# Kernel tuning notes

Measured on AMD Instinct MI355X. Metric: run time of the kernel, lower is better.

The kernel has to match this reference:

```python
import jax, jax.numpy as jnp
import numpy as np

EMBED_DIM = 1024
NUM_HEADS = 16
HEAD_DIM = EMBED_DIM // NUM_HEADS

# Hamilton-product combination tensor C[out_comp, weight_comp, in_comp]
_C = np.zeros((4, 4, 4), dtype=np.float32)
for o, terms in enumerate([
    [(0, 0, 1), (1, 1, -1), (2, 2, -1), (3, 3, -1)],  # r_out
    [(1, 0, 1), (0, 1, 1), (3, 2, 1), (2, 3, -1)],    # i_out
    [(2, 0, 1), (3, 1, -1), (0, 2, 1), (1, 3, 1)],    # j_out
    [(3, 0, 1), (2, 1, 1), (1, 2, -1), (0, 3, 1)],    # k_out
]):
    for d, c, s in terms:
        _C[o, d, c] = s
C = jnp.asarray(_C)


def _xavier(key, shape):
    fan_in, fan_out = shape[-1], shape[-2]
    a = jnp.sqrt(6.0 / (fan_in + fan_out))
    return jax.random.uniform(key, shape, jnp.float32, -a, a)


def setup_inputs() -> dict:
    key = jax.random.key(0)
    ks = jax.random.split(key, 8)
    B, T, E = 4, 1024, EMBED_DIM
    inp = {
        'q': jax.random.normal(ks[0], (B, T, E, 4), jnp.float32),
        'k': jax.random.normal(ks[1], (B, T, E, 4), jnp.float32),
        'v': jax.random.normal(ks[2], (B, T, E, 4), jnp.float32),
    }
    for name, kk in zip(['Wq', 'Wk', 'Wv', 'Wo'], ks[3:7]):
        # stacked [r,i,j,k] weights, each (out_features, in_features)
        inp[name] = _xavier(kk, (4, E, E))
        inp[name.replace('W', 'b')] = jnp.zeros((E, 4), jnp.float32)
    return inp


def qlinear(x, W, b):
    # x: [B,T,in,4(c)], W: [4(d),out,in], b: [out,4]
    # effective block weight: Weff[q_out, c_in, out, in]
    Weff = jnp.einsum('doi,qdc->qcoi', W, C)
    out = jnp.einsum('btic,qcoi->btoq', x, Weff)
    return out + b  # bias broadcasts over B,T


def split_heads(x):
    B, T, D, Q = x.shape
    x = x.reshape(B, T, NUM_HEADS, HEAD_DIM, Q)
    return x.transpose(0, 2, 1, 3, 4)  # [B,H,T,hd,4]


def combine_heads(x):
    B, H, T, D, Q = x.shape
    return x.transpose(0, 2, 1, 3, 4).reshape(B, T, H * D, Q)


def reference(q, k, v, Wq, bq, Wk, bk, Wv, bv, Wo, bo):
    qh = split_heads(qlinear(q, Wq, bq))
    kh = split_heads(qlinear(k, Wk, bk))
    vh = split_heads(qlinear(v, Wv, bv))
    scale = 1.0 / jnp.sqrt(jnp.float32(HEAD_DIM * 4))
    scores = jnp.einsum('bhqfd,bhkfd->bhqk', qh, kh) * scale
    attn = jax.nn.softmax(scores, axis=-1)
    out = jnp.einsum('bhqk,bhkfd->bhqfd', attn, vh)
    return qlinear(combine_heads(out), Wo, bo)
```

## Files before the change

### kernel.cpp

```cpp
#include <hip/hip_runtime.h>
#include <hip/hip_bf16.h>

typedef _Float16 h16;
typedef h16   h16x8 __attribute__((ext_vector_type(8)));
typedef h16   h16x4 __attribute__((ext_vector_type(4)));
typedef float f32x4 __attribute__((ext_vector_type(4)));

#define EMB 1024
#define ED4 4096L

__device__ __forceinline__ void gload_lds16(const void* g, void* l) {
    __builtin_amdgcn_global_load_lds(
        (__attribute__((address_space(1))) void*)g,
        (__attribute__((address_space(3))) void*)l,
        16, 0, 0);
}

__global__ __launch_bounds__(256) void k_build_m(const float* __restrict__ W, h16* __restrict__ M) {
    int t = blockIdx.x * 256 + threadIdx.x;
    int i = t & 1023;
    int n = t >> 10;
    int o = n >> 2, q = n & 3;
    unsigned packed = 0xEu | (0x8u << 4) | (0x2u << 8) | (0x4u << 12);
    unsigned sm = (packed >> (q * 4)) & 0xFu;
    h16x4 out;
#pragma unroll
    for (int c = 0; c < 4; ++c) {
        int d = q ^ c;
        float w = W[((long)d * EMB + o) * EMB + i];
        out[c] = (h16)(((sm >> c) & 1u) ? -w : w);
    }
    *(h16x4*)&M[(long)n * ED4 + i * 4] = out;
}

__global__ __launch_bounds__(256) void k_f32_to_f16(const float* __restrict__ in, h16* __restrict__ out) {
    long i = ((long)blockIdx.x * 256 + threadIdx.x) * 4;
    float4 v = *(const float4*)(in + i);
    h16x4 o;
    o[0] = (h16)v.x; o[1] = (h16)v.y; o[2] = (h16)v.z; o[3] = (h16)v.w;
    *(h16x4*)(out + i) = o;
}

#define BAR() __builtin_amdgcn_s_barrier()
#define LGKM0() do { asm volatile("s_waitcnt lgkmcnt(0)" ::: "memory"); \
                     __builtin_amdgcn_sched_barrier(0); } while (0)
#define STAGE(matv, basev, row0v, tt, hh) do { \
    const h16* _src = (basev) + ((row0v) + (hh) * 128L) * 4096L + (long)(tt) * 64 + scol; \
    h16* _dst = &lds[(((tt) & 1) << 15) + (matv) * 16384 + (hh) * 8192 + w * 512]; \
    gload_lds16(_src, _dst); \
    gload_lds16(_src + 64 * 4096L, _dst + 4096); \
} while (0)
#define LDA_(m, ks) (*(const h16x8*)&lds[cb + wm * 8192 + ((m) * 16 + fr) * 64 + ((((ks) * 4 + kq) ^ fr7) << 3)])
#define LDB_(n, ks) (*(const h16x8*)&lds[cb + 16384 + (wn >> 1) * 8192 + (((wn & 1) * 64) + (n) * 16 + fr) * 64 + ((((ks) * 4 + kq) ^ fr7) << 3)])

template <typename OUT_T>
__global__ __launch_bounds__(512, 2) void k_gemm256(
    const h16* __restrict__ A, const h16* __restrict__ B,
    OUT_T* __restrict__ C, const float* __restrict__ bias, int nt)
{
    __shared__ __align__(16) h16 lds[65536];

    const int tid = threadIdx.x;
    const int w  = tid >> 6, l = tid & 63;
    const int wm = w >> 2, wn = w & 3;
    const int fr = l & 15, fr7 = l & 7, kq = l >> 4;

    const int srow = w * 8 + (l >> 3);
    const int scol = ((l & 7) ^ ((l >> 3) & 7)) << 3;
    const long arow0 = (long)blockIdx.x * 256 + srow;
    const long brow0 = (long)blockIdx.y * 256 + srow;

    f32x4 acc[8][4] = {};

    STAGE(0, A, arow0, 0, 0);
    STAGE(0, A, arow0, 0, 1);
    STAGE(1, B, brow0, 0, 0);
    STAGE(1, B, brow0, 0, 1);
    STAGE(0, A, arow0, 1, 0);
    STAGE(0, A, arow0, 1, 1);
    STAGE(1, B, brow0, 1, 0);
    STAGE(1, B, brow0, 1, 1);
    asm volatile("s_waitcnt vmcnt(8)" ::: "memory");
    __builtin_amdgcn_sched_barrier(0);
    BAR();

    for (int t = 0; t < nt; ++t) {
        const int cb = (t & 1) << 15;
        h16x8 alo[4][2], ahi[4][2], bf[4][2];

#pragma unroll
        for (int m = 0; m < 4; ++m) { alo[m][0] = LDA_(m, 0); alo[m][1] = LDA_(m, 1); }
#pragma unroll
        for (int n = 0; n < 2; ++n) { bf[n][0] = LDB_(n, 0); bf[n][1] = LDB_(n, 1); }
        BAR(); LGKM0();
        __builtin_amdgcn_s_setprio(1);
#pragma unroll
        for (int m = 0; m < 4; ++m)
#pragma unroll
            for (int n = 0; n < 2; ++n) {
                acc[m][n] = __builtin_amdgcn_mfma_f32_16x16x32_f16(alo[m][0], bf[n][0], acc[m][n], 0, 0, 0);
                acc[m][n] = __builtin_amdgcn_mfma_f32_16x16x32_f16(alo[m][1], bf[n][1], acc[m][n], 0, 0, 0);
            }
        __builtin_amdgcn_s_setprio(0);
        BAR();

#pragma unroll
        for (int n = 2; n < 4; ++n) { bf[n][0] = LDB_(n, 0); bf[n][1] = LDB_(n, 1); }
        BAR(); LGKM0();
        __builtin_amdgcn_s_setprio(1);
#pragma unroll
        for (int m = 0; m < 4; ++m)
#pragma unroll
            for (int n = 2; n < 4; ++n) {
                acc[m][n] = __builtin_amdgcn_mfma_f32_16x16x32_f16(alo[m][0], bf[n][0], acc[m][n], 0, 0, 0);
                acc[m][n] = __builtin_amdgcn_mfma_f32_16x16x32_f16(alo[m][1], bf[n][1], acc[m][n], 0, 0, 0);
            }
        __builtin_amdgcn_s_setprio(0);
        BAR();

#pragma unroll
        for (int m = 0; m < 4; ++m) { ahi[m][0] = LDA_(m + 4, 0); ahi[m][1] = LDA_(m + 4, 1); }
        if (t + 2 < nt) {
            STAGE(1, B, brow0, t + 2, 0);
            STAGE(1, B, brow0, t + 2, 1);
        }
        BAR(); LGKM0();
        __builtin_amdgcn_s_setprio(1);
#pragma unroll
        for (int m = 0; m < 4; ++m)
#pragma unroll
            for (int n = 0; n < 2; ++n) {
                acc[m + 4][n] = __builtin_amdgcn_mfma_f32_16x16x32_f16(ahi[m][0], bf[n][0], acc[m + 4][n], 0, 0, 0);
                acc[m + 4][n] = __builtin_amdgcn_mfma_f32_16x16x32_f16(ahi[m][1], bf[n][1], acc[m + 4][n], 0, 0, 0);
            }
        __builtin_amdgcn_s_setprio(0);
        BAR();

        if (t + 2 < nt) {
            STAGE(0, A, arow0, t + 2, 0);
            STAGE(0, A, arow0, t + 2, 1);
        }
        if (t < nt - 2)       { asm volatile("s_waitcnt vmcnt(8)" ::: "memory"); }
        else                  { asm volatile("s_waitcnt vmcnt(0)" ::: "memory"); }
        __builtin_amdgcn_sched_barrier(0);
        BAR();
        __builtin_amdgcn_s_setprio(1);
#pragma unroll
        for (int m = 0; m < 4; ++m)
#pragma unroll
            for (int n = 2; n < 4; ++n) {
                acc[m + 4][n] = __builtin_amdgcn_mfma_f32_16x16x32_f16(ahi[m][0], bf[n][0], acc[m + 4][n], 0, 0, 0);
                acc[m + 4][n] = __builtin_amdgcn_mfma_f32_16x16x32_f16(ahi[m][1], bf[n][1], acc[m + 4][n], 0, 0, 0);
            }
        __builtin_amdgcn_s_setprio(0);
        BAR();
    }

    const long row0 = (long)blockIdx.x * 256 + wm * 128 + kq * 4;
    const int  col0 = (int)blockIdx.y * 256 + wn * 64 + fr;
#pragma unroll
    for (int n = 0; n < 4; ++n) {
        const int col = col0 + n * 16;
        const float bv = bias[col];
#pragma unroll
        for (int m = 0; m < 8; ++m) {
#pragma unroll
            for (int j = 0; j < 4; ++j)
                C[(row0 + m * 16 + j) * 4096L + col] = (OUT_T)(acc[m][n][j] + bv);
        }
    }
}

template <typename OUT_T, bool HAS_BIAS>
__global__ __launch_bounds__(256) void k_gemm_bt(
    const h16* __restrict__ A, const h16* __restrict__ B,
    OUT_T* __restrict__ C, const float* __restrict__ bias,
    int lda, int ldb, int ldc,
    long sAb, long sAh, long sBb, long sBh, long sCb, long sCh,
    float alpha, int kIters)
{
    __shared__ __align__(16) h16 As[128 * 32];
    __shared__ __align__(16) h16 Bs[128 * 32];

    const int z = blockIdx.z, zb = z >> 4, zh = z & 15;
    const h16* Ab = A + zb * sAb + zh * sAh + (long)blockIdx.x * 128 * lda;
    const h16* Bb = B + zb * sBb + zh * sBh + (long)blockIdx.y * 128 * ldb;

    const int tid = threadIdx.x, w = tid >> 6, lane = tid & 63;
    const int wr = (w >> 1) * 64, wc = (w & 1) * 64;
    const int scol = (lane & 3) * 8;
    const int srow = lane >> 2;
    const int koff = (lane >> 4) * 8;
    const int fr   = lane & 15;

    f32x4 acc[4][4] = {};

    for (int kt = 0; kt < kIters; ++kt) {
        const int k0 = kt * 32;
#pragma unroll
        for (int j = 0; j < 2; ++j) {
            const int ca  = w * 2 + j;
            const int row = ca * 16 + srow;
            gload_lds16(Ab + (long)row * lda + k0 + scol, &As[ca * 512]);
            gload_lds16(Bb + (long)row * ldb + k0 + scol, &Bs[ca * 512]);
        }
        __syncthreads();

        h16x8 af[4], bfr[4];
#pragma unroll
        for (int m = 0; m < 4; ++m)
            af[m] = *(const h16x8*)&As[(wr + m * 16 + fr) * 32 + koff];
#pragma unroll
        for (int n = 0; n < 4; ++n)
            bfr[n] = *(const h16x8*)&Bs[(wc + n * 16 + fr) * 32 + koff];
        __syncthreads();

#pragma unroll
        for (int m = 0; m < 4; ++m)
#pragma unroll
            for (int n = 0; n < 4; ++n)
                acc[m][n] = __builtin_amdgcn_mfma_f32_16x16x32_f16(af[m], bfr[n], acc[m][n], 0, 0, 0);
    }

    OUT_T* Cb = C + zb * sCb + zh * sCh;
    const long rbase = (long)blockIdx.x * 128 + wr + (lane >> 4) * 4;
    const int  cbase = blockIdx.y * 128 + wc + fr;
#pragma unroll
    for (int n = 0; n < 4; ++n) {
        const int col = cbase + n * 16;
        const float bv = HAS_BIAS ? bias[col] : 0.0f;
#pragma unroll
        for (int m = 0; m < 4; ++m) {
            const long row0 = rbase + m * 16;
#pragma unroll
            for (int j = 0; j < 4; ++j) {
                float vv = acc[m][n][j] * alpha + bv;
                Cb[(row0 + j) * ldc + col] = (OUT_T)vv;
            }
        }
    }
}

__global__ void k_transpose_v(const h16* __restrict__ Vb, h16* __restrict__ Vt) {
    __shared__ h16 tile[32][34];
    const int z = blockIdx.z, b = z >> 4, h = z & 15;
    const int f0 = blockIdx.x * 32, t0 = blockIdx.y * 32;
    const int tx = threadIdx.x, ty = threadIdx.y;
#pragma unroll
    for (int j = 0; j < 4; ++j)
        tile[ty + 8 * j][tx] = Vb[(long)(b * 1024 + t0 + ty + 8 * j) * ED4 + h * 256 + f0 + tx];
    __syncthreads();
#pragma unroll
    for (int j = 0; j < 4; ++j)
        Vt[(long)z * (256 * 1024) + (long)(f0 + ty + 8 * j) * 1024 + t0 + tx] = tile[tx][ty + 8 * j];
}

__global__ __launch_bounds__(256) void k_softmax(h16* __restrict__ S) {
    const long row = blockIdx.x;
    h16* p = S + row * 1024;
    const int tid = threadIdx.x, w = tid >> 6, lane = tid & 63;
    h16x4 xi = *(const h16x4*)&p[tid * 4];
    float x[4];
#pragma unroll
    for (int j = 0; j < 4; ++j) x[j] = (float)xi[j];
    float m = fmaxf(fmaxf(x[0], x[1]), fmaxf(x[2], x[3]));
#pragma unroll
    for (int off = 32; off; off >>= 1) m = fmaxf(m, __shfl_xor(m, off));
    __shared__ float red[8];
    if (lane == 0) red[w] = m;
    __syncthreads();
    m = fmaxf(fmaxf(red[0], red[1]), fmaxf(red[2], red[3]));
    float s = 0.0f;
#pragma unroll
    for (int j = 0; j < 4; ++j) { x[j] = __expf(x[j] - m); s += x[j]; }
#pragma unroll
    for (int off = 32; off; off >>= 1) s += __shfl_xor(s, off);
    if (lane == 0) red[4 + w] = s;
    __syncthreads();
    s = red[4] + red[5] + red[6] + red[7];
    const float inv = 1.0f / s;
    h16x4 o;
#pragma unroll
    for (int j = 0; j < 4; ++j) o[j] = (h16)(x[j] * inv);
    *(h16x4*)&p[tid * 4] = o;
}

extern "C" void kernel_launch(void* const* d_in, const int* in_sizes, int n_in,
                              void* d_out, int out_size, void* d_ws, size_t ws_size,
                              hipStream_t stream) {
    const float* q  = (const float*)d_in[0];
    const float* k  = (const float*)d_in[1];
    const float* v  = (const float*)d_in[2];
    const float* Wq = (const float*)d_in[3];
    const float* bq = (const float*)d_in[4];
    const float* Wk = (const float*)d_in[5];
    const float* bk = (const float*)d_in[6];
    const float* Wv = (const float*)d_in[7];
    const float* bv = (const float*)d_in[8];
    const float* Wo = (const float*)d_in[9];
    const float* bo = (const float*)d_in[10];
    float* out = (float*)d_out;

    char* ws = (char*)d_ws;
    const long MB = 1024L * 1024;
    h16* X  = (h16*)(ws + 0 * MB);
    h16* M  = (h16*)(ws + 32 * MB);
    h16* Qb = (h16*)(ws + 64 * MB);
    h16* Kb = (h16*)(ws + 96 * MB);
    h16* Vb = (h16*)(ws + 128 * MB);
    h16* Vt = (h16*)(ws + 160 * MB);
    h16* AO = (h16*)(ws + 192 * MB);
    h16* Sc = (h16*)(ws + 224 * MB);

    dim3 blk(256);
    dim3 g256(16, 16, 1);

    k_f32_to_f16<<<16384, blk, 0, stream>>>(q, X);
    k_build_m<<<16384, blk, 0, stream>>>(Wq, M);
    k_gemm256<h16><<<g256, 512, 0, stream>>>(X, M, Qb, bq, 64);

    k_f32_to_f16<<<16384, blk, 0, stream>>>(k, X);
    k_build_m<<<16384, blk, 0, stream>>>(Wk, M);
    k_gemm256<h16><<<g256, 512, 0, stream>>>(X, M, Kb, bk, 64);

    k_f32_to_f16<<<16384, blk, 0, stream>>>(v, X);
    k_build_m<<<16384, blk, 0, stream>>>(Wv, M);
    k_gemm256<h16><<<g256, 512, 0, stream>>>(X, M, Vb, bv, 64);

    k_transpose_v<<<dim3(8, 32, 64), dim3(32, 8), 0, stream>>>(Vb, Vt);

    for (int c = 0; c < 4; ++c) {
        const h16* Qc  = Qb + (long)c * 1024 * 4096;
        const h16* Kc  = Kb + (long)c * 1024 * 4096;
        const h16* VtC = Vt + (long)c * 16 * 256 * 1024;
        h16*       AOc = AO + (long)c * 1024 * 4096;

        k_gemm_bt<h16, false><<<dim3(8, 8, 16), blk, 0, stream>>>(
            Qc, Kc, Sc, nullptr,
            4096, 4096, 1024,
            0, 256,
            0, 256,
            0, 1024L * 1024,
            0.0625f, 8);

        k_softmax<<<16384, blk, 0, stream>>>(Sc);

        k_gemm_bt<h16, false><<<dim3(8, 2, 16), blk, 0, stream>>>(
            Sc, VtC, AOc, nullptr,
            1024, 1024, 4096,
            0, 1024L * 1024,
            0, 256L * 1024,
            0, 256,
            1.0f, 32);
    }

    k_build_m<<<16384, blk, 0, stream>>>(Wo, M);
    k_gemm256<float><<<g256, 512, 0, stream>>>(AO, M, out, bo, 64);
}
```

Baseline: 917.9 us.

## Remap warp tiles to quadrant layout and stage half-tiles as soon as freed

Each warp's 128x64 output tile is re-laid out as four 64x32 quadrants, one in each 128-row A half and 128-column B half of the block tile. Each warp now reads only one A half and one B half at a time. The global-to-LDS loads are spread across the four MFMA phases, so each half-tile of the next stages is issued as soon as its LDS half is no longer needed, with a tighter vmcnt wait. The aim is finer overlap of loads with compute and fewer bursts of outstanding loads, at the cost of more complex buffer-reuse timing, where a hazard could corrupt data.

```diff
diff --git a/kernel.cpp b/kernel.cpp
--- a/kernel.cpp
+++ b/kernel.cpp
@@ -50,8 +50,19 @@
     gload_lds16(_src, _dst); \
     gload_lds16(_src + 64 * 4096L, _dst + 4096); \
 } while (0)
-#define LDA_(m, ks) (*(const h16x8*)&lds[cb + wm * 8192 + ((m) * 16 + fr) * 64 + ((((ks) * 4 + kq) ^ fr7) << 3)])
-#define LDB_(n, ks) (*(const h16x8*)&lds[cb + 16384 + (wn >> 1) * 8192 + (((wn & 1) * 64) + (n) * 16 + fr) * 64 + ((((ks) * 4 + kq) ^ fr7) << 3)])
+#define LDA_(mh, m, ks) (*(const h16x8*)&lds[cb + (mh) * 8192 + (wm * 64 + (m) * 16 + fr) * 64 + ((((ks) * 4 + kq) ^ fr7) << 3)])
+#define LDB_(nh, n, ks) (*(const h16x8*)&lds[cb + 16384 + (nh) * 8192 + (wn * 32 + (n) * 16 + fr) * 64 + ((((ks) * 4 + kq) ^ fr7) << 3)])
+#define MFMA_Q(MH, NH, BF) do { \
+    __builtin_amdgcn_s_setprio(1); \
+    _Pragma("unroll") \
+    for (int m = 0; m < 4; ++m) \
+        _Pragma("unroll") \
+        for (int n = 0; n < 2; ++n) { \
+            acc[MH][NH][m][n] = __builtin_amdgcn_mfma_f32_16x16x32_f16(af[m][0], BF[n][0], acc[MH][NH][m][n], 0, 0, 0); \
+            acc[MH][NH][m][n] = __builtin_amdgcn_mfma_f32_16x16x32_f16(af[m][1], BF[n][1], acc[MH][NH][m][n], 0, 0, 0); \
+        } \
+    __builtin_amdgcn_s_setprio(0); \
+} while (0)
 
 template <typename OUT_T>
 __global__ __launch_bounds__(512, 2) void k_gemm256(
@@ -70,105 +81,72 @@
     const long arow0 = (long)blockIdx.x * 256 + srow;
     const long brow0 = (long)blockIdx.y * 256 + srow;
 
-    f32x4 acc[8][4] = {};
+    f32x4 acc[2][2][4][2] = {};
 
     STAGE(0, A, arow0, 0, 0);
+    STAGE(1, B, brow0, 0, 0);
     STAGE(0, A, arow0, 0, 1);
-    STAGE(1, B, brow0, 0, 0);
     STAGE(1, B, brow0, 0, 1);
     STAGE(0, A, arow0, 1, 0);
-    STAGE(0, A, arow0, 1, 1);
     STAGE(1, B, brow0, 1, 0);
-    STAGE(1, B, brow0, 1, 1);
-    asm volatile("s_waitcnt vmcnt(8)" ::: "memory");
+    asm volatile("s_waitcnt vmcnt(4)" ::: "memory");
     __builtin_amdgcn_sched_barrier(0);
     BAR();
 
     for (int t = 0; t < nt; ++t) {
         const int cb = (t & 1) << 15;
-        h16x8 alo[4][2], ahi[4][2], bf[4][2];
-
-#pragma unroll
-        for (int m = 0; m < 4; ++m) { alo[m][0] = LDA_(m, 0); alo[m][1] = LDA_(m, 1); }
-#pragma unroll
-        for (int n = 0; n < 2; ++n) { bf[n][0] = LDB_(n, 0); bf[n][1] = LDB_(n, 1); }
+        h16x8 af[4][2], b0[2][2], b1[2][2];
+
+#pragma unroll
+        for (int m = 0; m < 4; ++m) { af[m][0] = LDA_(0, m, 0); af[m][1] = LDA_(0, m, 1); }
+#pragma unroll
+        for (int n = 0; n < 2; ++n) { b0[n][0] = LDB_(0, n, 0); b0[n][1] = LDB_(0, n, 1); }
+        if (t + 1 < nt) STAGE(0, A, arow0, t + 1, 1);
         BAR(); LGKM0();
-        __builtin_amdgcn_s_setprio(1);
-#pragma unroll
-        for (int m = 0; m < 4; ++m)
+        MFMA_Q(0, 0, b0);
+        BAR();
+
+#pragma unroll
+        for (int n = 0; n < 2; ++n) { b1[n][0] = LDB_(1, n, 0); b1[n][1] = LDB_(1, n, 1); }
+        if (t + 1 < nt) STAGE(1, B, brow0, t + 1, 1);
+        BAR(); LGKM0();
+        MFMA_Q(0, 1, b1);
+        BAR();
+
+#pragma unroll
+        for (int m = 0; m < 4; ++m) { af[m][0] = LDA_(1, m, 0); af[m][1] = LDA_(1, m, 1); }
+        if (t + 2 < nt) STAGE(0, A, arow0, t + 2, 0);
+        BAR(); LGKM0();
+        MFMA_Q(1, 0, b0);
+        BAR();
+
+        if (t + 2 < nt) STAGE(1, B, brow0, t + 2, 0);
+        if (t < nt - 2) { asm volatile("s_waitcnt vmcnt(4)" ::: "memory"); }
+        else            { asm volatile("s_waitcnt vmcnt(0)" ::: "memory"); }
+        __builtin_amdgcn_sched_barrier(0);
+        BAR();
+        MFMA_Q(1, 1, b1);
+        BAR();
+    }
+
+    const long row00 = (long)blockIdx.x * 256 + wm * 64 + kq * 4;
+    const int  col00 = (int)blockIdx.y * 256 + wn * 32 + fr;
+#pragma unroll
+    for (int mh = 0; mh < 2; ++mh)
+#pragma unroll
+        for (int nh = 0; nh < 2; ++nh)
 #pragma unroll
             for (int n = 0; n < 2; ++n) {
-                acc[m][n] = __builtin_amdgcn_mfma_f32_16x16x32_f16(alo[m][0], bf[n][0], acc[m][n], 0, 0, 0);
-                acc[m][n] = __builtin_amdgcn_mfma_f32_16x16x32_f16(alo[m][1], bf[n][1], acc[m][n], 0, 0, 0);
+                const int col = col00 + nh * 128 + n * 16;
+                const float bv = bias[col];
+#pragma unroll
+                for (int m = 0; m < 4; ++m) {
+                    const long r0 = row00 + mh * 128 + m * 16;
+#pragma unroll
+                    for (int j = 0; j < 4; ++j)
+                        C[(r0 + j) * 4096L + col] = (OUT_T)(acc[mh][nh][m][n][j] + bv);
+                }
             }
-        __builtin_amdgcn_s_setprio(0);
-        BAR();
-
-#pragma unroll
-        for (int n = 2; n < 4; ++n) { bf[n][0] = LDB_(n, 0); bf[n][1] = LDB_(n, 1); }
-        BAR(); LGKM0();
-        __builtin_amdgcn_s_setprio(1);
-#pragma unroll
-        for (int m = 0; m < 4; ++m)
-#pragma unroll
-            for (int n = 2; n < 4; ++n) {
-                acc[m][n] = __builtin_amdgcn_mfma_f32_16x16x32_f16(alo[m][0], bf[n][0], acc[m][n], 0, 0, 0);
-                acc[m][n] = __builtin_amdgcn_mfma_f32_16x16x32_f16(alo[m][1], bf[n][1], acc[m][n], 0, 0, 0);
-            }
-        __builtin_amdgcn_s_setprio(0);
-        BAR();
-
-#pragma unroll
-        for (int m = 0; m < 4; ++m) { ahi[m][0] = LDA_(m + 4, 0); ahi[m][1] = LDA_(m + 4, 1); }
-        if (t + 2 < nt) {
-            STAGE(1, B, brow0, t + 2, 0);
-            STAGE(1, B, brow0, t + 2, 1);
-        }
-        BAR(); LGKM0();
-        __builtin_amdgcn_s_setprio(1);
-#pragma unroll
-        for (int m = 0; m < 4; ++m)
-#pragma unroll
-            for (int n = 0; n < 2; ++n) {
-                acc[m + 4][n] = __builtin_amdgcn_mfma_f32_16x16x32_f16(ahi[m][0], bf[n][0], acc[m + 4][n], 0, 0, 0);
-                acc[m + 4][n] = __builtin_amdgcn_mfma_f32_16x16x32_f16(ahi[m][1], bf[n][1], acc[m + 4][n], 0, 0, 0);
-            }
-        __builtin_amdgcn_s_setprio(0);
-        BAR();
-
-        if (t + 2 < nt) {
-            STAGE(0, A, arow0, t + 2, 0);
-            STAGE(0, A, arow0, t + 2, 1);
-        }
-        if (t < nt - 2)       { asm volatile("s_waitcnt vmcnt(8)" ::: "memory"); }
-        else                  { asm volatile("s_waitcnt vmcnt(0)" ::: "memory"); }
-        __builtin_amdgcn_sched_barrier(0);
-        BAR();
-        __builtin_amdgcn_s_setprio(1);
-#pragma unroll
-        for (int m = 0; m < 4; ++m)
-#pragma unroll
-            for (int n = 2; n < 4; ++n) {
-                acc[m + 4][n] = __builtin_amdgcn_mfma_f32_16x16x32_f16(ahi[m][0], bf[n][0], acc[m + 4][n], 0, 0, 0);
-                acc[m + 4][n] = __builtin_amdgcn_mfma_f32_16x16x32_f16(ahi[m][1], bf[n][1], acc[m + 4][n], 0, 0, 0);
-            }
-        __builtin_amdgcn_s_setprio(0);
-        BAR();
-    }
-
-    const long row0 = (long)blockIdx.x * 256 + wm * 128 + kq * 4;
-    const int  col0 = (int)blockIdx.y * 256 + wn * 64 + fr;
-#pragma unroll
-    for (int n = 0; n < 4; ++n) {
-        const int col = col0 + n * 16;
-        const float bv = bias[col];
-#pragma unroll
-        for (int m = 0; m < 8; ++m) {
-#pragma unroll
-            for (int j = 0; j < 4; ++j)
-                C[(row0 + m * 16 + j) * 4096L + col] = (OUT_T)(acc[m][n][j] + bv);
-        }
-    }
 }
 
 template <typename OUT_T, bool HAS_BIAS>
```

Measured after the change: 908.7 us. Within noise of the previous version (-1.0%).
